# Optimization experiments

Hardware: AMD Instinct MI355X
Metric: run time of the kernel (lower is better)

Reference implementation:

```python
import jax, jax.numpy as jnp
import numpy as np

B, T1, T2, D, H = 16, 512, 64, 768, 12
E = D // H  # head dim


def _proj(x, W, b):
    # x: [B,T,D], W: [6,D,D], b: [6,D] -> [6,B,H,T,E], scaled by E**-0.25 (applied to q,k,v alike, per source)
    t = x.shape[1]
    p = jnp.einsum('btd,kdf->kbtf', x, W) + b[:, None, None, :]
    p = p.reshape(6, B, t, H, E).transpose(0, 1, 3, 2, 4)
    return p * (E ** -0.25)


def setup_inputs() -> dict:
    key = jax.random.key(0)
    ks = jax.random.split(key, 12)
    s = 0.02
    return {
        'feats': jax.random.normal(ks[0], (B, T1, D), jnp.float32),
        'inps': jax.random.normal(ks[1], (B, T2, D), jnp.float32),
        'att_mask': jax.random.randint(ks[2], (B, 1, 1, T1 + T2), 0, 2).astype(bool),
        'W_f': s * jax.random.normal(ks[3], (6, D, D), jnp.float32),
        'b_f': s * jax.random.normal(ks[4], (6, D), jnp.float32),
        'W_i': s * jax.random.normal(ks[5], (6, D, D), jnp.float32),
        'b_i': s * jax.random.normal(ks[6], (6, D), jnp.float32),
        'Wu_v': s * jax.random.normal(ks[7], (D, D), jnp.float32),
        'bu_v': s * jax.random.normal(ks[8], (D,), jnp.float32),
        'Wu_l': s * jax.random.normal(ks[9], (D, D), jnp.float32),
        'bu_l': s * jax.random.normal(ks[10], (D,), jnp.float32),
    }


def reference(feats, inps, att_mask, W_f, b_f, W_i, b_i, Wu_v, bu_v, Wu_l, bu_l):
    NEG = jnp.float32(-1e9)
    # projections from feats: [keys_v_v, queries_v_v, values_v_v, queries_l_v, keys_v_l, values_v_l]
    k_vv, q_vv, v_vv, q_lv, k_vl, v_vl = _proj(feats, W_f, b_f)
    # projections from inps: [keys_l_v, values_l_v, queries_v_l, queries_l_l, keys_l_l, values_l_l]
    k_lv, v_lv, q_vl, q_ll, k_ll, v_ll = _proj(inps, W_i, b_i)

    # visual stream: two distinct queries over the two key blocks, joint softmax over t1+t2
    dot_vv = jnp.einsum('bhqe,bhke->bhqk', q_vv, k_vv)   # [B,H,T1,T1]
    dot_lv = jnp.einsum('bhqe,bhke->bhqk', q_lv, k_lv)   # [B,H,T1,T2]
    att_v = jnp.concatenate([dot_vv, dot_lv], axis=-1)    # [B,H,T1,T1+T2]
    att_v = jax.nn.softmax(jnp.where(att_mask, NEG, att_v), axis=-1)
    vals_v = jnp.concatenate([v_vv, v_lv], axis=2)        # [B,H,T1+T2,E]
    out_v = jnp.einsum('bhqk,bhke->bhqe', att_v, vals_v)
    out_v = out_v.transpose(0, 2, 1, 3).reshape(B, T1, D)
    out_v = out_v @ Wu_v + bu_v

    # language stream
    dot_vl = jnp.einsum('bhqe,bhke->bhqk', q_vl, k_vl)    # [B,H,T2,T1]
    dot_ll = jnp.einsum('bhqe,bhke->bhqk', q_ll, k_ll)    # [B,H,T2,T2]
    att_l = jnp.concatenate([dot_vl, dot_ll], axis=-1)    # [B,H,T2,T1+T2]
    att_l = jax.nn.softmax(jnp.where(att_mask, NEG, att_l), axis=-1)
    vals_l = jnp.concatenate([v_vl, v_ll], axis=2)        # [B,H,T1+T2,E]
    out_l = jnp.einsum('bhqk,bhke->bhqe', att_l, vals_l)
    out_l = out_l.transpose(0, 2, 1, 3).reshape(B, T2, D)
    out_l = out_l @ Wu_l + bu_l

    return (out_v, out_l)
```

## Files before the change

kernel.cpp:

```cpp
#include <hip/hip_runtime.h>
#include <stdint.h>

#define BB 16
#define T1C 512
#define T2C 64
#define DC 768
#define HC 12
#define EC 64
#define SC 576
#define QSCALE 0.35355339059327379f

typedef __attribute__((ext_vector_type(8))) short bf16x8;
typedef __attribute__((ext_vector_type(4))) float f32x4;

__device__ __forceinline__ uint16_t f2b(float f) {
    union { float f; uint32_t i; } v; v.f = f;
    return (uint16_t)((v.i + 0x7fffu + ((v.i >> 16) & 1u)) >> 16);
}
__device__ __forceinline__ uint16_t f2bfast(float f) {
    union { float f; uint32_t i; } v; v.f = f;
    return (uint16_t)((v.i + 0x8000u) >> 16);
}
__device__ __forceinline__ uint32_t pk2(float a, float b) {
    return (uint32_t)f2b(a) | ((uint32_t)f2b(b) << 16);
}

__device__ __forceinline__ void gll16(const void* g, void* l) {
    __builtin_amdgcn_global_load_lds(
        (const __attribute__((address_space(1))) uint32_t*)(uintptr_t)g,
        (__attribute__((address_space(3))) uint32_t*)(uintptr_t)l, 16, 0, 0);
}

#define WT_BLOCKS (24 * 24 * 14)
#define XS_BLOCKS 3456

__global__ __launch_bounds__(256) void prep(
    const float* __restrict__ Wf, const float* __restrict__ Wi,
    const float* __restrict__ Wuv, const float* __restrict__ Wul,
    uint16_t* __restrict__ Wt,
    const float* __restrict__ Xf, const float* __restrict__ Xi,
    uint16_t* __restrict__ Of, uint16_t* __restrict__ Oi,
    const uint32_t* __restrict__ mw, int* __restrict__ flags)
{
    __shared__ union { float tile[32][33]; int d[3]; } sh;
    const int bid = blockIdx.x;
    if (bid < WT_BLOCKS) {
        const int z = bid / 576, r = bid % 576;
        const int kx = r % 24, fy = r / 24;
        const float* src = (z < 6)  ? Wf + (size_t)z * DC * DC
                         : (z < 12) ? Wi + (size_t)(z - 6) * DC * DC
                         : (z == 12 ? Wuv : Wul);
        uint16_t* dst = Wt + (size_t)z * DC * DC;
        const int tx = threadIdx.x & 31, ty = threadIdx.x >> 5;
        const int k0 = kx * 32, f0 = fy * 32;
#pragma unroll
        for (int q = 0; q < 4; q++)
            sh.tile[ty + q * 8][tx] = src[(size_t)(k0 + ty + q * 8) * DC + f0 + tx];
        __syncthreads();
        if (threadIdx.x < 128) {
            const int fl = threadIdx.x & 31, kg = threadIdx.x >> 5;
            const int p = (f0 + fl) >> 4, rlid = fl & 15;
            uint4 o;
            o.x = pk2(sh.tile[kg * 8 + 0][fl], sh.tile[kg * 8 + 1][fl]);
            o.y = pk2(sh.tile[kg * 8 + 2][fl], sh.tile[kg * 8 + 3][fl]);
            o.z = pk2(sh.tile[kg * 8 + 4][fl], sh.tile[kg * 8 + 5][fl]);
            o.w = pk2(sh.tile[kg * 8 + 6][fl], sh.tile[kg * 8 + 7][fl]);
            *(uint4*)(dst + ((size_t)((p * 24 + kx) * 4 + kg) * 16 + rlid) * 8) = o;
        }
    } else if (bid < WT_BLOCKS + XS_BLOCKS) {
        const int nf = BB * T1C * DC / 8;
        const int ni = BB * T2C * DC / 8;
        int t = (bid - WT_BLOCKS) * 256 + threadIdx.x;
        const float* src; uint16_t* dst; int cc;
        if (t < nf) { src = Xf; dst = Of; cc = t; }
        else        { cc = t - nf; if (cc >= ni) return; src = Xi; dst = Oi; }
        int rlid = cc & 15;
        int t2 = cc >> 4;
        int qd = t2 & 3;
        int t3 = t2 >> 2;
        int kt = t3 % 24;
        int p  = t3 / 24;
        const float* sp = src + (size_t)(p * 16 + rlid) * DC + kt * 32 + qd * 8;
        float4 a = *(const float4*)sp;
        float4 b = *(const float4*)(sp + 4);
        uint4 o;
        o.x = pk2(a.x, a.y); o.y = pk2(a.z, a.w);
        o.z = pk2(b.x, b.y); o.w = pk2(b.z, b.w);
        *(uint4*)(dst + (size_t)cc * 8) = o;
    } else {
        if (threadIdx.x == 0) { sh.d[0] = 0; sh.d[1] = 0; sh.d[2] = 0; }
        __syncthreads();
        int lW = 0, lB = 0, lL = 0;
        for (int i = threadIdx.x; i < 2304; i += 256) {
            uint32_t w = mw[i];
            if (w > 1u) lW = 1;
            if (((w) & 0xffu) > 1u || ((w >> 8) & 0xffu) > 1u ||
                ((w >> 16) & 0xffu) > 1u || ((w >> 24) & 0xffu) > 1u) lB = 1;
            if ((w & 0xffffu) > 1u) lL = 1;
        }
        if (lW) atomicOr(&sh.d[0], 1);
        if (lB) atomicOr(&sh.d[1], 1);
        if (lL) atomicOr(&sh.d[2], 1);
        __syncthreads();
        if (threadIdx.x == 0)
            flags[0] = (!sh.d[0]) ? 0 : ((!sh.d[1]) ? 1 : (sh.d[2] ? 2 : 0));
    }
}

#define BSTR 76

__global__ __launch_bounds__(256, 2) void gemm_proj_mfma(
    const uint16_t* __restrict__ Xsf, const uint16_t* __restrict__ Xsi,
    const uint16_t* __restrict__ Wt,
    const float* __restrict__ b_f, const float* __restrict__ b_i,
    uint16_t* __restrict__ Pf, uint16_t* __restrict__ Pi)
{
    __shared__ union {
        struct { uint16_t A[2][128 * 32]; uint16_t B[2][256 * 32]; } st;
        uint16_t bounce[4][16 * BSTR];
    } sm;
    const int tid = threadIdx.x;
    const int w = tid >> 6, l = tid & 63;
    const bool isf = (blockIdx.x < 64);
    const int mx = isf ? blockIdx.x : blockIdx.x - 64;
    const int m0 = mx * 128;
    const int T  = isf ? T1C : T2C;
    const uint16_t* Xs = isf ? Xsf : Xsi;
    const float* bias  = isf ? b_f : b_i;
    uint16_t* P        = isf ? Pf : Pi;
    const int vmask    = isf ? 0x24 : 0x22;
    const int k6 = blockIdx.y / 3, nb = blockIdx.y % 3;
    const int n0 = nb * 256;
    const uint16_t* Bsrc = Wt + (size_t)((isf ? 0 : 6) + k6) * DC * DC;

    const int lid = l & 15, qd = l >> 4;
    const int wm = w >> 1, wn = w & 1;

    f32x4 acc[4][8] = {};

    const uint16_t* sA0 = Xs + ((size_t)((mx * 8 + w * 2 + 0) * 24) * 64 + l) * 8;
    const uint16_t* sA1 = Xs + ((size_t)((mx * 8 + w * 2 + 1) * 24) * 64 + l) * 8;
    const uint16_t* sB0 = Bsrc + ((size_t)((nb * 16 + w * 4 + 0) * 24) * 64 + l) * 8;
    const uint16_t* sB1 = Bsrc + ((size_t)((nb * 16 + w * 4 + 1) * 24) * 64 + l) * 8;
    const uint16_t* sB2 = Bsrc + ((size_t)((nb * 16 + w * 4 + 2) * 24) * 64 + l) * 8;
    const uint16_t* sB3 = Bsrc + ((size_t)((nb * 16 + w * 4 + 3) * 24) * 64 + l) * 8;

#define PJ_STAGE(bu) { \
        gll16(sA0, &sm.st.A[bu][(w * 2 + 0) * 512]); sA0 += 512; \
        gll16(sA1, &sm.st.A[bu][(w * 2 + 1) * 512]); sA1 += 512; \
        gll16(sB0, &sm.st.B[bu][(w * 4 + 0) * 512]); sB0 += 512; \
        gll16(sB1, &sm.st.B[bu][(w * 4 + 1) * 512]); sB1 += 512; \
        gll16(sB2, &sm.st.B[bu][(w * 4 + 2) * 512]); sB2 += 512; \
        gll16(sB3, &sm.st.B[bu][(w * 4 + 3) * 512]); sB3 += 512; }
#define PJ_C(bu) { bf16x8 aq[4], bq[8]; \
        _Pragma("unroll") for (int i = 0; i < 4; i++) \
            aq[i] = *(const bf16x8*)&sm.st.A[bu][((wm * 4 + i) * 64 + l) * 8]; \
        _Pragma("unroll") for (int j = 0; j < 8; j++) \
            bq[j] = *(const bf16x8*)&sm.st.B[bu][((wn * 8 + j) * 64 + l) * 8]; \
        _Pragma("unroll") for (int i = 0; i < 4; i++) \
        _Pragma("unroll") for (int j = 0; j < 8; j++) \
            acc[i][j] = __builtin_amdgcn_mfma_f32_16x16x32_bf16(aq[i], bq[j], acc[i][j], 0, 0, 0); }

    PJ_STAGE(0);

    for (int k2 = 0; k2 < 12; ++k2) {
        __builtin_amdgcn_s_barrier();
        __builtin_amdgcn_sched_barrier(0);
        PJ_STAGE(1);
        asm volatile("s_waitcnt vmcnt(6)" ::: "memory");
        __builtin_amdgcn_sched_barrier(0);
        __builtin_amdgcn_s_barrier();
        __builtin_amdgcn_sched_barrier(0);
        PJ_C(0);
        __builtin_amdgcn_s_barrier();
        __builtin_amdgcn_sched_barrier(0);
        if (k2 < 11) {
            PJ_STAGE(0);
            asm volatile("s_waitcnt vmcnt(6)" ::: "memory");
        } else {
            asm volatile("s_waitcnt vmcnt(0)" ::: "memory");
        }
        __builtin_amdgcn_sched_barrier(0);
        __builtin_amdgcn_s_barrier();
        __builtin_amdgcn_sched_barrier(0);
        PJ_C(1);
    }
#undef PJ_STAGE
#undef PJ_C

    float bv[8];
#pragma unroll
    for (int j = 0; j < 8; j++)
        bv[j] = bias[k6 * DC + n0 + wn * 128 + j * 16 + lid];
    __syncthreads();

    uint16_t* reg = sm.bounce[w];
    const int mb = m0 + wm * 64;
    const int b = mb / T, tb = mb - b * T;
    const int rrow = l >> 2;
    const int rcol = (l & 3) * 16;

    if (!((vmask >> k6) & 1)) {
#pragma unroll
        for (int hl = 0; hl < 2; hl++) {
            const int h = nb * 4 + wn * 2 + hl;
            uint16_t* dst0 = P + ((((size_t)k6 * BB + b) * HC + h) * T + tb + rrow) * EC + rcol;
#pragma unroll
            for (int p = 0; p < 4; p++) {
#pragma unroll
                for (int jj = 0; jj < 4; jj++)
#pragma unroll
                    for (int r = 0; r < 4; r++)
                        reg[(qd * 4 + r) * BSTR + jj * 16 + lid] =
                            f2b((acc[p][hl * 4 + jj][r] + bv[hl * 4 + jj]) * QSCALE);
                uint4 d0 = *(const uint4*)&reg[rrow * BSTR + rcol];
                uint4 d1 = *(const uint4*)&reg[rrow * BSTR + rcol + 8];
                uint16_t* dst = dst0 + (size_t)p * 16 * EC;
                *(uint4*)dst = d0;
                *(uint4*)(dst + 8) = d1;
            }
        }
    } else {
#pragma unroll
        for (int hl = 0; hl < 2; hl++) {
            const int h = nb * 4 + wn * 2 + hl;
            uint16_t* dst0 = P + (size_t)k6 * BB * HC * T * EC
                               + (((size_t)b * HC + h) * EC + rrow) * T + tb + rcol;
#pragma unroll
            for (int p = 0; p < 4; p++) {
#pragma unroll
                for (int i = 0; i < 4; i++) {
                    uint32_t w0 = pk2((acc[i][hl * 4 + p][0] + bv[hl * 4 + p]) * QSCALE,
                                      (acc[i][hl * 4 + p][1] + bv[hl * 4 + p]) * QSCALE);
                    uint32_t w1 = pk2((acc[i][hl * 4 + p][2] + bv[hl * 4 + p]) * QSCALE,
                                      (acc[i][hl * 4 + p][3] + bv[hl * 4 + p]) * QSCALE);
                    *(uint2*)&reg[lid * BSTR + i * 16 + qd * 4] = make_uint2(w0, w1);
                }
                uint4 d0 = *(const uint4*)&reg[rrow * BSTR + rcol];
                uint4 d1 = *(const uint4*)&reg[rrow * BSTR + rcol + 8];
                uint16_t* dst = dst0 + (size_t)p * 16 * T;
                *(uint4*)dst = d0;
                *(uint4*)(dst + 8) = d1;
            }
        }
    }
}

__global__ __launch_bounds__(256, 4) void gemm_out_mfma(
    const uint16_t* __restrict__ Osv, const uint16_t* __restrict__ Osl,
    const uint16_t* __restrict__ Wt,
    const float* __restrict__ bu_v, const float* __restrict__ bu_l,
    float* __restrict__ out)
{
    __shared__ struct { uint16_t A[2][128 * 32]; uint16_t B[2][128 * 32]; } st;
    const int tid = threadIdx.x;
    const int w = tid >> 6, l = tid & 63;
    const bool isv = (blockIdx.x < 64);
    const int mx = isv ? blockIdx.x : blockIdx.x - 64;
    const int m0 = mx * 128;
    const int rowoff = isv ? 0 : BB * T1C;
    const uint16_t* A = isv ? Osv : Osl;
    const uint16_t* Wtm = Wt + (size_t)(isv ? 12 : 13) * DC * DC;
    const float* bias = isv ? bu_v : bu_l;
    const int n0 = blockIdx.y * 128;
    const int lid = l & 15, qd = l >> 4;
    const int wm = w >> 1, wn = w & 1;
    const int c0 = w * 2;

    f32x4 acc[4][4] = {};

    const uint16_t* sA0 = A + ((size_t)((mx * 8 + c0 + 0) * 24) * 64 + l) * 8;
    const uint16_t* sA1 = A + ((size_t)((mx * 8 + c0 + 1) * 24) * 64 + l) * 8;
    const uint16_t* sB0 = Wtm + ((size_t)((blockIdx.y * 8 + c0 + 0) * 24) * 64 + l) * 8;
    const uint16_t* sB1 = Wtm + ((size_t)((blockIdx.y * 8 + c0 + 1) * 24) * 64 + l) * 8;

#define GO_STAGE(bu) { \
        gll16(sA0, &st.A[bu][(c0 + 0) * 512]); sA0 += 512; \
        gll16(sA1, &st.A[bu][(c0 + 1) * 512]); sA1 += 512; \
        gll16(sB0, &st.B[bu][(c0 + 0) * 512]); sB0 += 512; \
        gll16(sB1, &st.B[bu][(c0 + 1) * 512]); sB1 += 512; }
#define GO_C(bu) { bf16x8 aq[4], bq[4]; \
        _Pragma("unroll") for (int i = 0; i < 4; i++) \
            aq[i] = *(const bf16x8*)&st.A[bu][((wm * 4 + i) * 64 + l) * 8]; \
        _Pragma("unroll") for (int j = 0; j < 4; j++) \
            bq[j] = *(const bf16x8*)&st.B[bu][((wn * 4 + j) * 64 + l) * 8]; \
        _Pragma("unroll") for (int i = 0; i < 4; i++) \
        _Pragma("unroll") for (int j = 0; j < 4; j++) \
            acc[i][j] = __builtin_amdgcn_mfma_f32_16x16x32_bf16(aq[i], bq[j], acc[i][j], 0, 0, 0); }

    GO_STAGE(0);

    for (int k2 = 0; k2 < 12; ++k2) {
        __builtin_amdgcn_s_barrier();
        __builtin_amdgcn_sched_barrier(0);
        GO_STAGE(1);
        asm volatile("s_waitcnt vmcnt(4)" ::: "memory");
        __builtin_amdgcn_sched_barrier(0);
        __builtin_amdgcn_s_barrier();
        __builtin_amdgcn_sched_barrier(0);
        GO_C(0);
        __builtin_amdgcn_s_barrier();
        __builtin_amdgcn_sched_barrier(0);
        if (k2 < 11) {
            GO_STAGE(0);
            asm volatile("s_waitcnt vmcnt(4)" ::: "memory");
        } else {
            asm volatile("s_waitcnt vmcnt(0)" ::: "memory");
        }
        __builtin_amdgcn_sched_barrier(0);
        __builtin_amdgcn_s_barrier();
        __builtin_amdgcn_sched_barrier(0);
        GO_C(1);
    }
#undef GO_STAGE
#undef GO_C

    float bv[4];
#pragma unroll
    for (int j = 0; j < 4; j++)
        bv[j] = bias[n0 + wn * 64 + j * 16 + lid];
#pragma unroll
    for (int i = 0; i < 4; i++)
#pragma unroll
        for (int j = 0; j < 4; j++)
#pragma unroll
            for (int r = 0; r < 4; r++) {
                int m = m0 + wm * 64 + i * 16 + qd * 4 + r;
                int f = n0 + wn * 64 + j * 16 + lid;
                out[(size_t)(rowoff + m) * DC + f] = acc[i][j][r] + bv[j];
            }
}

__global__ __launch_bounds__(256, 3) void attn_mfma(
    const uint16_t* __restrict__ Pf,
    const uint16_t* __restrict__ Pi,
    const void* __restrict__ maskp,
    const int* __restrict__ flags,
    uint16_t* __restrict__ Osv,
    uint16_t* __restrict__ Osl)
{
    __shared__ uint16_t Klds[64 * 72];
    __shared__ uint16_t Vlds[64 * 72];
    __shared__ uint16_t Plds[4][16 * 72];
    __shared__ float    Ma[SC];
    __shared__ float    Lw[4][16];

    const int bh = blockIdx.x;
    const int tile = blockIdx.y;
    const int b = bh / HC, h = bh % HC;
    const int tid = threadIdx.x;
    const int w = tid >> 6, l = tid & 63;
    const int lid = l & 15, qd = l >> 4;

    const size_t SF = (size_t)BB * HC * T1C * EC;
    const size_t SI = (size_t)BB * HC * T2C * EC;

    const bool vis = (tile < 8);
    const uint16_t *Qa, *Qb, *K1, *K2, *V1, *V2;
    uint16_t* O; int Tq, q0;
    if (vis) { Qa = Pf + 1 * SF; Qb = Pf + 3 * SF; K1 = Pf;          K2 = Pi;
               V1 = Pf + 2 * SF; V2 = Pi + 1 * SI; O = Osv; Tq = T1C; q0 = tile * 64; }
    else     { Qa = Pi + 2 * SI; Qb = Pi + 3 * SI; K1 = Pf + 4 * SF; K2 = Pi + 4 * SI;
               V1 = Pf + 5 * SF; V2 = Pi + 5 * SI; O = Osl; Tq = T2C; q0 = 0; }

    {
        const int kind = flags[0];
        for (int i = tid; i < SC; i += 256) {
            int idx = b * SC + i;
            int mv;
            if (kind == 0)      mv = ((const uint32_t*)maskp)[idx] != 0u;
            else if (kind == 1) mv = ((const uint8_t*)maskp)[idx] != 0;
            else                mv = ((const uint16_t*)maskp)[idx] != 0;
            Ma[i] = mv ? -1e9f : 0.0f;
        }
    }

    const int q = q0 + w * 16 + lid;
    const uint16_t* Qrow  = Qa + ((size_t)bh * Tq + q) * EC;
    const uint16_t* Qrow2 = Qb + ((size_t)bh * Tq + q) * EC;
    bf16x8 qf0 = *(const bf16x8*)(Qrow + qd * 8);
    bf16x8 qf1 = *(const bf16x8*)(Qrow + 32 + qd * 8);
    bf16x8 qg0 = *(const bf16x8*)(Qrow2 + qd * 8);
    bf16x8 qg1 = *(const bf16x8*)(Qrow2 + 32 + qd * 8);

    f32x4 o[4];
#pragma unroll
    for (int ef = 0; ef < 4; ef++) { o[ef][0]=0.f; o[ef][1]=0.f; o[ef][2]=0.f; o[ef][3]=0.f; }
    float u[4] = {0.f, 0.f, 0.f, 0.f};

    const int skey = tid >> 2, se0 = (tid & 3) * 16;
    const int ve = tid >> 2,  vc = tid & 3;

    auto kptr = [&](int c) -> const uint16_t* {
        return (c < 8) ? K1 + ((size_t)bh * T1C + c * 64 + skey) * EC + se0
                       : K2 + ((size_t)bh * T2C + skey) * EC + se0;
    };
    auto vptr = [&](int c) -> const uint16_t* {
        return (c < 8) ? V1 + ((size_t)bh * EC + ve) * T1C + c * 64 + vc * 16
                       : V2 + ((size_t)bh * EC + ve) * T2C + vc * 16;
    };

    uint4 ka0 = *(const uint4*)kptr(0);
    uint4 ka1 = *(const uint4*)(kptr(0) + 8);
    uint4 va0 = *(const uint4*)vptr(0);
    uint4 va1 = *(const uint4*)(vptr(0) + 8);

#pragma unroll
    for (int c = 0; c < 9; ++c) {
        uint4 kb0, kb1, vb0, vb1;
        if (c < 8) {
            kb0 = *(const uint4*)kptr(c + 1);
            kb1 = *(const uint4*)(kptr(c + 1) + 8);
            vb0 = *(const uint4*)vptr(c + 1);
            vb1 = *(const uint4*)(vptr(c + 1) + 8);
        }
        __builtin_amdgcn_s_barrier();
        __builtin_amdgcn_sched_barrier(0);
        *(uint4*)&Klds[skey * 72 + se0]         = ka0;
        *(uint4*)&Klds[skey * 72 + se0 + 8]     = ka1;
        *(uint4*)&Vlds[ve * 72 + vc * 16]       = va0;
        *(uint4*)&Vlds[ve * 72 + vc * 16 + 8]   = va1;
        asm volatile("s_waitcnt lgkmcnt(0)" ::: "memory");
        __builtin_amdgcn_sched_barrier(0);
        __builtin_amdgcn_s_barrier();
        __builtin_amdgcn_sched_barrier(0);

        const int k0 = c * 64;
        const bf16x8 q_0 = (c < 8) ? qf0 : qg0;
        const bf16x8 q_1 = (c < 8) ? qf1 : qg1;
        f32x4 s[4];
#pragma unroll
        for (int sub = 0; sub < 4; sub++) {
            bf16x8 kf0 = *(const bf16x8*)&Klds[(sub * 16 + lid) * 72 + qd * 8];
            bf16x8 kf1 = *(const bf16x8*)&Klds[(sub * 16 + lid) * 72 + 32 + qd * 8];
            f32x4 z; z[0]=0.f; z[1]=0.f; z[2]=0.f; z[3]=0.f;
            z = __builtin_amdgcn_mfma_f32_16x16x32_bf16(q_0, kf0, z, 0, 0, 0);
            s[sub] = __builtin_amdgcn_mfma_f32_16x16x32_bf16(q_1, kf1, z, 0, 0, 0);
        }
#pragma unroll
        for (int sub = 0; sub < 4; sub++) {
            float mv = Ma[k0 + sub * 16 + lid];
#pragma unroll
            for (int r = 0; r < 4; r++) {
                float p = __expf(s[sub][r] + mv);
                u[r] += p;
                Plds[w][(qd * 4 + r) * 72 + sub * 16 + lid] = f2bfast(p);
            }
        }
#pragma unroll
        for (int half = 0; half < 2; half++) {
            bf16x8 pf = *(const bf16x8*)&Plds[w][lid * 72 + half * 32 + qd * 8];
#pragma unroll
            for (int ef = 0; ef < 4; ef++) {
                bf16x8 vf = *(const bf16x8*)&Vlds[(ef * 16 + lid) * 72 + half * 32 + qd * 8];
                o[ef] = __builtin_amdgcn_mfma_f32_16x16x32_bf16(vf, pf, o[ef], 0, 0, 0);
            }
        }
        if (c < 8) { ka0 = kb0; ka1 = kb1; va0 = vb0; va1 = vb1; }
    }

#pragma unroll
    for (int d = 1; d <= 8; d <<= 1)
#pragma unroll
        for (int r = 0; r < 4; r++)
            u[r] += __shfl_xor(u[r], d, 64);
    if (lid == 0) {
#pragma unroll
        for (int r = 0; r < 4; r++) Lw[w][qd * 4 + r] = u[r];
    }
    float rl = 1.f / Lw[w][lid];

    const size_t p = ((size_t)b * Tq + q0 + w * 16) >> 4;
#pragma unroll
    for (int ef = 0; ef < 4; ef++) {
        uint32_t w0 = pk2(o[ef][0] * rl, o[ef][1] * rl);
        uint32_t w1 = pk2(o[ef][2] * rl, o[ef][3] * rl);
        size_t chunk = ((p * 24 + h * 2 + (ef >> 1)) * 4 + (ef & 1) * 2 + (qd >> 1)) * 16 + lid;
        *(uint2*)(O + chunk * 8 + (qd & 1) * 4) = make_uint2(w0, w1);
    }
}

extern "C" void kernel_launch(void* const* d_in, const int* in_sizes, int n_in,
                              void* d_out, int out_size, void* d_ws, size_t ws_size,
                              hipStream_t stream)
{
    const float* feats = (const float*)d_in[0];
    const float* inps  = (const float*)d_in[1];
    const void*  maskp = d_in[2];
    const float* W_f   = (const float*)d_in[3];
    const float* b_f   = (const float*)d_in[4];
    const float* W_i   = (const float*)d_in[5];
    const float* b_i   = (const float*)d_in[6];
    const float* Wu_v  = (const float*)d_in[7];
    const float* bu_v  = (const float*)d_in[8];
    const float* Wu_l  = (const float*)d_in[9];
    const float* bu_l  = (const float*)d_in[10];

    const size_t MAT = (size_t)DC * DC;
    const size_t PF_E = 6ull * BB * HC * T1C * EC;
    const size_t PI_E = 6ull * BB * HC * T2C * EC;
    uint16_t* Wt  = (uint16_t*)d_ws;
    uint16_t* Osv = Wt;
    uint16_t* Osl = Wt + (size_t)BB * T1C * HC * EC;
    uint16_t* Pf  = Wt + 14 * MAT;
    uint16_t* Pi  = Pf + PF_E;
    int* flags    = (int*)(Pi + PI_E);

    uint16_t* Xsf = (uint16_t*)d_out;
    uint16_t* Xsi = Xsf + (size_t)BB * T1C * DC;

    prep<<<dim3(WT_BLOCKS + XS_BLOCKS + 1), dim3(256), 0, stream>>>(
        W_f, W_i, Wu_v, Wu_l, Wt, feats, inps, Xsf, Xsi,
        (const uint32_t*)maskp, flags);

    gemm_proj_mfma<<<dim3(72, 18), dim3(256), 0, stream>>>(
        Xsf, Xsi, Wt, b_f, b_i, Pf, Pi);

    attn_mfma<<<dim3(BB * HC, 9), dim3(256), 0, stream>>>(
        Pf, Pi, maskp, flags, Osv, Osl);

    gemm_out_mfma<<<dim3(72, 6), dim3(256), 0, stream>>>(
        Osv, Osl, Wt, bu_v, bu_l, (float*)d_out);
}
```

Baseline: 257.4 us.

## Triple-buffer LDS staging in projection and output GEMMs with one barrier per step

Both MFMA GEMM kernels move from double-buffered to triple-buffered LDS staging. The k-loop is restructured so each step issues one wait plus barrier, then prefetches two tiles ahead while computing the current tile. This is meant to hide global-load latency and remove one barrier per tile. In exchange it uses more LDS: the output GEMM's launch bounds drop from 4 to 3 blocks per CU, and the projection GEMM may lose occupancy too.

```diff
diff --git a/kernel.cpp b/kernel.cpp
--- a/kernel.cpp
+++ b/kernel.cpp
@@ -116,7 +116,7 @@
     uint16_t* __restrict__ Pf, uint16_t* __restrict__ Pi)
 {
     __shared__ union {
-        struct { uint16_t A[2][128 * 32]; uint16_t B[2][256 * 32]; } st;
+        struct { uint16_t A[3][128 * 32]; uint16_t B[3][256 * 32]; } st;
         uint16_t bounce[4][16 * BSTR];
     } sm;
     const int tid = threadIdx.x;
@@ -160,33 +160,35 @@
         _Pragma("unroll") for (int i = 0; i < 4; i++) \
         _Pragma("unroll") for (int j = 0; j < 8; j++) \
             acc[i][j] = __builtin_amdgcn_mfma_f32_16x16x32_bf16(aq[i], bq[j], acc[i][j], 0, 0, 0); }
-
-    PJ_STAGE(0);
-
-    for (int k2 = 0; k2 < 12; ++k2) {
-        __builtin_amdgcn_s_barrier();
-        __builtin_amdgcn_sched_barrier(0);
-        PJ_STAGE(1);
-        asm volatile("s_waitcnt vmcnt(6)" ::: "memory");
-        __builtin_amdgcn_sched_barrier(0);
-        __builtin_amdgcn_s_barrier();
-        __builtin_amdgcn_sched_barrier(0);
+#define PJ_SYNC(N) { \
+        asm volatile("s_waitcnt vmcnt(" #N ")" ::: "memory"); \
+        __builtin_amdgcn_sched_barrier(0); \
+        __builtin_amdgcn_s_barrier(); \
+        __builtin_amdgcn_sched_barrier(0); }
+
+    PJ_STAGE(0); PJ_STAGE(1);
+
+    for (int k3 = 0; k3 < 8; ++k3) {
+        PJ_SYNC(6);
+        PJ_STAGE(2);
         PJ_C(0);
-        __builtin_amdgcn_s_barrier();
-        __builtin_amdgcn_sched_barrier(0);
-        if (k2 < 11) {
+        if (k3 < 7) {
+            PJ_SYNC(6);
             PJ_STAGE(0);
-            asm volatile("s_waitcnt vmcnt(6)" ::: "memory");
+            PJ_C(1);
+            PJ_SYNC(6);
+            PJ_STAGE(1);
+            PJ_C(2);
         } else {
-            asm volatile("s_waitcnt vmcnt(0)" ::: "memory");
-        }
-        __builtin_amdgcn_sched_barrier(0);
-        __builtin_amdgcn_s_barrier();
-        __builtin_amdgcn_sched_barrier(0);
-        PJ_C(1);
+            PJ_SYNC(6);
+            PJ_C(1);
+            PJ_SYNC(0);
+            PJ_C(2);
+        }
     }
 #undef PJ_STAGE
 #undef PJ_C
+#undef PJ_SYNC
 
     float bv[8];
 #pragma unroll
@@ -246,13 +248,13 @@
     }
 }
 
-__global__ __launch_bounds__(256, 4) void gemm_out_mfma(
+__global__ __launch_bounds__(256, 3) void gemm_out_mfma(
     const uint16_t* __restrict__ Osv, const uint16_t* __restrict__ Osl,
     const uint16_t* __restrict__ Wt,
     const float* __restrict__ bu_v, const float* __restrict__ bu_l,
     float* __restrict__ out)
 {
-    __shared__ struct { uint16_t A[2][128 * 32]; uint16_t B[2][128 * 32]; } st;
+    __shared__ struct { uint16_t A[3][128 * 32]; uint16_t B[3][128 * 32]; } st;
     const int tid = threadIdx.x;
     const int w = tid >> 6, l = tid & 63;
     const bool isv = (blockIdx.x < 64);
@@ -287,33 +289,35 @@
         _Pragma("unroll") for (int i = 0; i < 4; i++) \
         _Pragma("unroll") for (int j = 0; j < 4; j++) \
             acc[i][j] = __builtin_amdgcn_mfma_f32_16x16x32_bf16(aq[i], bq[j], acc[i][j], 0, 0, 0); }
-
-    GO_STAGE(0);
-
-    for (int k2 = 0; k2 < 12; ++k2) {
-        __builtin_amdgcn_s_barrier();
-        __builtin_amdgcn_sched_barrier(0);
-        GO_STAGE(1);
-        asm volatile("s_waitcnt vmcnt(4)" ::: "memory");
-        __builtin_amdgcn_sched_barrier(0);
-        __builtin_amdgcn_s_barrier();
-        __builtin_amdgcn_sched_barrier(0);
+#define GO_SYNC(N) { \
+        asm volatile("s_waitcnt vmcnt(" #N ")" ::: "memory"); \
+        __builtin_amdgcn_sched_barrier(0); \
+        __builtin_amdgcn_s_barrier(); \
+        __builtin_amdgcn_sched_barrier(0); }
+
+    GO_STAGE(0); GO_STAGE(1);
+
+    for (int k3 = 0; k3 < 8; ++k3) {
+        GO_SYNC(4);
+        GO_STAGE(2);
         GO_C(0);
-        __builtin_amdgcn_s_barrier();
-        __builtin_amdgcn_sched_barrier(0);
-        if (k2 < 11) {
+        if (k3 < 7) {
+            GO_SYNC(4);
             GO_STAGE(0);
-            asm volatile("s_waitcnt vmcnt(4)" ::: "memory");
+            GO_C(1);
+            GO_SYNC(4);
+            GO_STAGE(1);
+            GO_C(2);
         } else {
-            asm volatile("s_waitcnt vmcnt(0)" ::: "memory");
-        }
-        __builtin_amdgcn_sched_barrier(0);
-        __builtin_amdgcn_s_barrier();
-        __builtin_amdgcn_sched_barrier(0);
-        GO_C(1);
+            GO_SYNC(4);
+            GO_C(1);
+            GO_SYNC(0);
+            GO_C(2);
+        }
     }
 #undef GO_STAGE
 #undef GO_C
+#undef GO_SYNC
 
     float bv[4];
 #pragma unroll
```

After: 255.1 us. No clear change (-0.9%).

## Double-buffer K/V shared memory tiles to drop one barrier per chunk

Applied to the files above, without the earlier changes.

The attention kernel now keeps two LDS buffers for the K and V tiles. Each iteration stores the next chunk into the alternate buffer while computing on the current one, and it prefetches global loads two chunks ahead. This replaces two barriers per iteration with one and overlaps LDS writes with MFMA work. The cost is doubled K/V LDS usage, which may reduce occupancy under launch_bounds(256,3), plus extra registers held for the deeper prefetch.

```diff
diff --git a/kernel.cpp b/kernel.cpp
--- a/kernel.cpp
+++ b/kernel.cpp
@@ -339,8 +339,8 @@
     uint16_t* __restrict__ Osv,
     uint16_t* __restrict__ Osl)
 {
-    __shared__ uint16_t Klds[64 * 72];
-    __shared__ uint16_t Vlds[64 * 72];
+    __shared__ uint16_t Klds[2][64 * 72];
+    __shared__ uint16_t Vlds[2][64 * 72];
     __shared__ uint16_t Plds[4][16 * 72];
     __shared__ float    Ma[SC];
     __shared__ float    Lw[4][16];
@@ -390,6 +390,8 @@
 
     const int skey = tid >> 2, se0 = (tid & 3) * 16;
     const int ve = tid >> 2,  vc = tid & 3;
+    const uint32_t ko = skey * 72 + se0;
+    const uint32_t vo = ve * 72 + vc * 16;
 
     auto kptr = [&](int c) -> const uint16_t* {
         return (c < 8) ? K1 + ((size_t)bh * T1C + c * 64 + skey) * EC + se0
@@ -400,30 +402,40 @@
                        : V2 + ((size_t)bh * EC + ve) * T2C + vc * 16;
     };
 
-    uint4 ka0 = *(const uint4*)kptr(0);
-    uint4 ka1 = *(const uint4*)(kptr(0) + 8);
-    uint4 va0 = *(const uint4*)vptr(0);
-    uint4 va1 = *(const uint4*)(vptr(0) + 8);
+    {
+        uint4 t0 = *(const uint4*)kptr(0);
+        uint4 t1 = *(const uint4*)(kptr(0) + 8);
+        uint4 t2 = *(const uint4*)vptr(0);
+        uint4 t3 = *(const uint4*)(vptr(0) + 8);
+        *(uint4*)&Klds[0][ko]     = t0;
+        *(uint4*)&Klds[0][ko + 8] = t1;
+        *(uint4*)&Vlds[0][vo]     = t2;
+        *(uint4*)&Vlds[0][vo + 8] = t3;
+    }
+    uint4 ka0 = *(const uint4*)kptr(1);
+    uint4 ka1 = *(const uint4*)(kptr(1) + 8);
+    uint4 va0 = *(const uint4*)vptr(1);
+    uint4 va1 = *(const uint4*)(vptr(1) + 8);
+    asm volatile("s_waitcnt lgkmcnt(0)" ::: "memory");
+    __builtin_amdgcn_s_barrier();
+    __builtin_amdgcn_sched_barrier(0);
 
 #pragma unroll
     for (int c = 0; c < 9; ++c) {
+        const int cb = c & 1, nx = cb ^ 1;
+        if (c < 8) {
+            *(uint4*)&Klds[nx][ko]     = ka0;
+            *(uint4*)&Klds[nx][ko + 8] = ka1;
+            *(uint4*)&Vlds[nx][vo]     = va0;
+            *(uint4*)&Vlds[nx][vo + 8] = va1;
+        }
         uint4 kb0, kb1, vb0, vb1;
-        if (c < 8) {
-            kb0 = *(const uint4*)kptr(c + 1);
-            kb1 = *(const uint4*)(kptr(c + 1) + 8);
-            vb0 = *(const uint4*)vptr(c + 1);
-            vb1 = *(const uint4*)(vptr(c + 1) + 8);
-        }
-        __builtin_amdgcn_s_barrier();
-        __builtin_amdgcn_sched_barrier(0);
-        *(uint4*)&Klds[skey * 72 + se0]         = ka0;
-        *(uint4*)&Klds[skey * 72 + se0 + 8]     = ka1;
-        *(uint4*)&Vlds[ve * 72 + vc * 16]       = va0;
-        *(uint4*)&Vlds[ve * 72 + vc * 16 + 8]   = va1;
-        asm volatile("s_waitcnt lgkmcnt(0)" ::: "memory");
-        __builtin_amdgcn_sched_barrier(0);
-        __builtin_amdgcn_s_barrier();
-        __builtin_amdgcn_sched_barrier(0);
+        if (c < 7) {
+            kb0 = *(const uint4*)kptr(c + 2);
+            kb1 = *(const uint4*)(kptr(c + 2) + 8);
+            vb0 = *(const uint4*)vptr(c + 2);
+            vb1 = *(const uint4*)(vptr(c + 2) + 8);
+        }
 
         const int k0 = c * 64;
         const bf16x8 q_0 = (c < 8) ? qf0 : qg0;
@@ -431,8 +443,8 @@
         f32x4 s[4];
 #pragma unroll
         for (int sub = 0; sub < 4; sub++) {
-            bf16x8 kf0 = *(const bf16x8*)&Klds[(sub * 16 + lid) * 72 + qd * 8];
-            bf16x8 kf1 = *(const bf16x8*)&Klds[(sub * 16 + lid) * 72 + 32 + qd * 8];
+            bf16x8 kf0 = *(const bf16x8*)&Klds[cb][(sub * 16 + lid) * 72 + qd * 8];
+            bf16x8 kf1 = *(const bf16x8*)&Klds[cb][(sub * 16 + lid) * 72 + 32 + qd * 8];
             f32x4 z; z[0]=0.f; z[1]=0.f; z[2]=0.f; z[3]=0.f;
             z = __builtin_amdgcn_mfma_f32_16x16x32_bf16(q_0, kf0, z, 0, 0, 0);
             s[sub] = __builtin_amdgcn_mfma_f32_16x16x32_bf16(q_1, kf1, z, 0, 0, 0);
@@ -452,11 +464,17 @@
             bf16x8 pf = *(const bf16x8*)&Plds[w][lid * 72 + half * 32 + qd * 8];
 #pragma unroll
             for (int ef = 0; ef < 4; ef++) {
-                bf16x8 vf = *(const bf16x8*)&Vlds[(ef * 16 + lid) * 72 + half * 32 + qd * 8];
+                bf16x8 vf = *(const bf16x8*)&Vlds[cb][(ef * 16 + lid) * 72 + half * 32 + qd * 8];
                 o[ef] = __builtin_amdgcn_mfma_f32_16x16x32_bf16(vf, pf, o[ef], 0, 0, 0);
             }
         }
-        if (c < 8) { ka0 = kb0; ka1 = kb1; va0 = vb0; va1 = vb1; }
+        if (c < 8) {
+            asm volatile("s_waitcnt lgkmcnt(0)" ::: "memory");
+            __builtin_amdgcn_sched_barrier(0);
+            __builtin_amdgcn_s_barrier();
+            __builtin_amdgcn_sched_barrier(0);
+        }
+        if (c < 7) { ka0 = kb0; ka1 = kb1; va0 = vb0; va1 = vb1; }
     }
 
 #pragma unroll
```

Result: faster. 249.9 us (-2.9%).
